# Kernel tuning notes

Measured on AMD Instinct MI355X. Metric: run time of the kernel, lower is better.

## Reference

```python
import math
import jax, jax.numpy as jnp
import numpy as np

BSZ, N_HEADS, N_KV_HEADS, SEQLEN, HEAD_DIM = 1, 32, 8, 2048, 128
DIM = N_HEADS * HEAD_DIM  # 4096
N_REP = N_HEADS // N_KV_HEADS  # 4
NEG = -1e9


def setup_inputs() -> dict:
    key = jax.random.key(0)
    kq, kk, kv = jax.random.split(key, 3)
    q = jax.random.normal(kq, (BSZ, N_HEADS, SEQLEN, HEAD_DIM), dtype=jnp.float32)
    k = jax.random.normal(kk, (BSZ, N_KV_HEADS, SEQLEN, HEAD_DIM), dtype=jnp.float32)
    v = jax.random.normal(kv, (BSZ, N_KV_HEADS, SEQLEN, HEAD_DIM), dtype=jnp.float32)
    # additive causal mask: 0 on/below diagonal, large negative above
    causal = jnp.tril(jnp.ones((SEQLEN, SEQLEN), dtype=bool))
    mask = jnp.where(causal, 0.0, NEG).astype(jnp.float32)
    input_pos = jnp.zeros((1,), dtype=jnp.int64)
    return {"input_pos": input_pos, "q": q, "k": k, "v": v,
            "bsz": BSZ, "seqlen": SEQLEN, "mask": mask}


def reference(input_pos, q, k, v, bsz, seqlen, mask):
    # repeat_kv: (b, n_kv, s, d) -> (b, n_kv*n_rep, s, d), repeat_interleave on head dim
    k = jnp.repeat(k, N_REP, axis=1)
    v = jnp.repeat(v, N_REP, axis=1)
    scale = 1.0 / math.sqrt(q.shape[-1])
    # (b, h, s, s)
    attn = jnp.einsum("bhqd,bhkd->bhqk", q, k) * scale + mask
    attn = jax.nn.softmax(attn, axis=-1)
    y = jnp.einsum("bhqk,bhkd->bhqd", attn, v)  # (b, h, s, d)
    return y.transpose(0, 2, 1, 3).reshape(bsz, seqlen, DIM)
```

## Files before the change

### kernel.cpp

```cpp
#include <hip/hip_runtime.h>
#include <hip/hip_bf16.h>

#define SEQ 2048
#define HD 128
#define NH 32
#define NKV 8
#define ODIM 4096
#define QB 64
#define KVB 64
#define SCALE 0.08838834764831845f
#define NEGBIG -1e9f

typedef __attribute__((ext_vector_type(8))) short bf16x8;
typedef __attribute__((ext_vector_type(4))) float f32x4;

__device__ __forceinline__ unsigned short f2bf(float x) {
  union { __hip_bfloat16 b; unsigned short u; } c;
  c.b = __float2bfloat16(x);
  return c.u;
}

__device__ __forceinline__ unsigned pack2bf(float lo, float hi) {
  union { __hip_bfloat162 h; unsigned u; } c;
  c.h = __float22bfloat162_rn(float2{lo, hi});
  return c.u;
}

__device__ __forceinline__ void gload_lds16(const unsigned char* g, unsigned char* l) {
  __builtin_amdgcn_global_load_lds(
      (const __attribute__((address_space(1))) void*)g,
      (__attribute__((address_space(3))) void*)l, 16, 0, 0);
}

#define KWORK (NKV * SEQ * 16)
#define VWORK (NKV * (SEQ / 2) * 16)
__global__ __launch_bounds__(256) void sdpa_prepass(
    const float* __restrict__ k, const float* __restrict__ v,
    unsigned char* __restrict__ ws) {
  unsigned char* kimg = ws;
  unsigned char* vimg = ws + (NKV * 32 * 16384);
  int idx = (int)blockIdx.x * 256 + (int)threadIdx.x;
  if (idx < KWORK) {
    int hkv = idx >> 15;
    int rem = idx & 32767;
    int rg = rem >> 4;
    int c8 = (rem & 15) << 3;
    const float* src = k + ((size_t)hkv * SEQ + rg) * HD + c8;
    float4 a = *(const float4*)(src);
    float4 b = *(const float4*)(src + 4);
    union { unsigned short hh[8]; uint4 u4; } pk;
    pk.hh[0]=f2bf(a.x); pk.hh[1]=f2bf(a.y); pk.hh[2]=f2bf(a.z); pk.hh[3]=f2bf(a.w);
    pk.hh[4]=f2bf(b.x); pk.hh[5]=f2bf(b.y); pk.hh[6]=f2bf(b.z); pk.hh[7]=f2bf(b.w);
    int t = rg >> 6, r = rg & 63;
    size_t base = ((size_t)(hkv * 32 + t)) << 14;
    *(uint4*)(kimg + base + (r << 8) + ((c8 << 1) ^ ((r & 7) << 4))) = pk.u4;
  } else {
    int u = idx - KWORK;
    if (u >= VWORK) return;
    int hkv = u >> 14;
    int rem = u & 16383;
    int pr = rem >> 4;
    int d0 = (rem & 15) << 3;
    int rg = pr << 1;
    const float* s0 = v + ((size_t)hkv * SEQ + rg) * HD + d0;
    const float* s1 = s0 + HD;
    float4 a0 = *(const float4*)(s0);
    float4 b0 = *(const float4*)(s0 + 4);
    float4 a1 = *(const float4*)(s1);
    float4 b1 = *(const float4*)(s1 + 4);
    float lo[8] = {a0.x,a0.y,a0.z,a0.w,b0.x,b0.y,b0.z,b0.w};
    float hi[8] = {a1.x,a1.y,a1.z,a1.w,b1.x,b1.y,b1.z,b1.w};
    int t = rg >> 6, rr = rg & 63;
    size_t base = ((size_t)(hkv * 32 + t)) << 14;
    int rb = rr << 1;
    #pragma unroll
    for (int j = 0; j < 8; ++j) {
      int d = d0 + j;
      *(unsigned*)(vimg + base + (d << 7) + (rb ^ ((d & 7) << 4))) =
          pack2bf(lo[j], hi[j]);
    }
  }
}

__global__ __launch_bounds__(512, 4) void sdpa_flash_kernel(
    const float* __restrict__ q, const unsigned char* __restrict__ kimg,
    const unsigned char* __restrict__ vimg, float* __restrict__ out) {
  __shared__ __align__(16) unsigned char smem[65536];
  const int tid = threadIdx.x;
  const int w = tid >> 6;
  const int l = tid & 63;
  const int lm = l & 15;
  const int lg = l >> 4;

  const int p = (int)blockIdx.x;
  const int qtA = p;
  const int qtB = 31 - p;
  const int myqt = (w < 4) ? qtA : qtB;
  const int h = (int)blockIdx.y;
  const int hkv = h >> 2;
  const int qbase = myqt * QB + 16 * (w & 3);
  const int myrow = qbase + lm;

  bf16x8 qa[4];
  {
    const float* qr = q + ((size_t)(h * SEQ + myrow)) * HD + 8 * lg;
    #pragma unroll
    for (int c = 0; c < 4; ++c) {
      float4 a = *(const float4*)(qr + 32 * c);
      float4 b = *(const float4*)(qr + 32 * c + 4);
      union { unsigned short hh[8]; bf16x8 vv; } pk;
      pk.hh[0] = f2bf(a.x * SCALE); pk.hh[1] = f2bf(a.y * SCALE);
      pk.hh[2] = f2bf(a.z * SCALE); pk.hh[3] = f2bf(a.w * SCALE);
      pk.hh[4] = f2bf(b.x * SCALE); pk.hh[5] = f2bf(b.y * SCALE);
      pk.hh[6] = f2bf(b.z * SCALE); pk.hh[7] = f2bf(b.w * SCALE);
      qa[c] = pk.vv;
    }
  }

  f32x4 o[8];
  #pragma unroll
  for (int i = 0; i < 8; ++i) o[i] = (f32x4){0.f, 0.f, 0.f, 0.f};
  float mrow = -1e30f;
  float lrow = 0.f;

  const int ntiles = qtB + 1;
  const unsigned char* kt0 = kimg + (((size_t)(hkv * 32)) << 14);
  const unsigned char* vt0 = vimg + (((size_t)(hkv * 32)) << 14);
  const int woff = w << 10;

#define STAGE(tt, bufbase) {                                                 \
    const unsigned char* ks_ = kt0 + (((size_t)(tt)) << 14);                 \
    const unsigned char* vs_ = vt0 + (((size_t)(tt)) << 14);                 \
    unsigned char* Kb_ = (bufbase);                                          \
    unsigned char* Vb_ = (bufbase) + 16384;                                  \
    gload_lds16(ks_ + woff + (l << 4), Kb_ + woff);                          \
    gload_lds16(ks_ + 8192 + woff + (l << 4), Kb_ + 8192 + woff);            \
    gload_lds16(vs_ + woff + (l << 4), Vb_ + woff);                          \
    gload_lds16(vs_ + 8192 + woff + (l << 4), Vb_ + 8192 + woff);            \
  }

  STAGE(0, smem);
  __syncthreads();
  int cur = 0;

  for (int t = 0; t < ntiles; ++t) {
    const int kv0 = t * KVB;
    if (t + 1 < ntiles) STAGE(t + 1, smem + ((cur ^ 1) << 15));

    unsigned char* Klds = smem + (cur << 15);
    unsigned char* Vlds = Klds + 16384;

    if (t <= myqt) {
      f32x4 s[4];
      #pragma unroll
      for (int nt = 0; nt < 4; ++nt) s[nt] = (f32x4){0.f, 0.f, 0.f, 0.f};
      __builtin_amdgcn_s_setprio(1);
      #pragma unroll
      for (int nt = 0; nt < 4; ++nt) {
        int r = (nt << 4) + lm;
        #pragma unroll
        for (int kc = 0; kc < 4; ++kc) {
          int byte = (r << 8) + (((kc << 6) + (lg << 4)) ^ ((r & 7) << 4));
          bf16x8 kb = *(const bf16x8*)(Klds + byte);
          s[nt] = __builtin_amdgcn_mfma_f32_16x16x32_bf16(kb, qa[kc], s[nt], 0, 0, 0);
        }
      }
      __builtin_amdgcn_s_setprio(0);

      if (kv0 + KVB - 1 > qbase) {
        #pragma unroll
        for (int nt = 0; nt < 4; ++nt) {
          #pragma unroll
          for (int i = 0; i < 4; ++i) {
            int col = kv0 + (nt << 4) + (lg << 2) + i;
            s[nt][i] += (col > myrow) ? NEGBIG : 0.f;
          }
        }
      }

      float tm = -1e30f;
      #pragma unroll
      for (int nt = 0; nt < 4; ++nt)
        #pragma unroll
        for (int i = 0; i < 4; ++i) tm = fmaxf(tm, s[nt][i]);
      tm = fmaxf(tm, __shfl_xor(tm, 16));
      tm = fmaxf(tm, __shfl_xor(tm, 32));
      float mn = fmaxf(mrow, tm);
      float fac = __expf(mrow - mn);
      mrow = mn;
      float rs = 0.f;
      #pragma unroll
      for (int nt = 0; nt < 4; ++nt) {
        #pragma unroll
        for (int i = 0; i < 4; ++i) {
          float pv = __expf(s[nt][i] - mn);
          s[nt][i] = pv;
          rs += pv;
        }
      }
      rs += __shfl_xor(rs, 16);
      rs += __shfl_xor(rs, 32);
      lrow = lrow * fac + rs;
      #pragma unroll
      for (int nt2 = 0; nt2 < 8; ++nt2) {
        #pragma unroll
        for (int i = 0; i < 4; ++i) o[nt2][i] *= fac;
      }

      unsigned pk0[4], pk1[4];
      #pragma unroll
      for (int nt = 0; nt < 4; ++nt) {
        pk0[nt] = pack2bf(s[nt][0], s[nt][1]);
        pk1[nt] = pack2bf(s[nt][2], s[nt][3]);
      }
      const int srcA = lm + ((lg & 1) << 5);
      const int srcB = srcA + 16;
      const bool lo2 = (lg < 2);
      bf16x8 pb[2];
      #pragma unroll
      for (int kc = 0; kc < 2; ++kc) {
        int a0 = __shfl((int)pk0[2*kc], srcA), b0 = __shfl((int)pk0[2*kc+1], srcA);
        int a1 = __shfl((int)pk1[2*kc], srcA), b1 = __shfl((int)pk1[2*kc+1], srcA);
        int a2 = __shfl((int)pk0[2*kc], srcB), b2 = __shfl((int)pk0[2*kc+1], srcB);
        int a3 = __shfl((int)pk1[2*kc], srcB), b3 = __shfl((int)pk1[2*kc+1], srcB);
        union { int uu[4]; bf16x8 v; } pw;
        pw.uu[0] = lo2 ? a0 : b0;
        pw.uu[1] = lo2 ? a1 : b1;
        pw.uu[2] = lo2 ? a2 : b2;
        pw.uu[3] = lo2 ? a3 : b3;
        pb[kc] = pw.v;
      }

      __builtin_amdgcn_s_setprio(1);
      #pragma unroll
      for (int nt2 = 0; nt2 < 8; ++nt2) {
        int dr = (nt2 << 4) + lm;
        #pragma unroll
        for (int kc = 0; kc < 2; ++kc) {
          int byte = (dr << 7) + (((kc << 6) + (lg << 4)) ^ ((dr & 7) << 4));
          bf16x8 vb = *(const bf16x8*)(Vlds + byte);
          o[nt2] = __builtin_amdgcn_mfma_f32_16x16x32_bf16(vb, pb[kc], o[nt2], 0, 0, 0);
        }
      }
      __builtin_amdgcn_s_setprio(0);
    }

    __syncthreads();
    cur ^= 1;
  }

  float inv = 1.f / lrow;
  float* orow = out + (size_t)myrow * ODIM + h * HD + (lg << 2);
  #pragma unroll
  for (int nt2 = 0; nt2 < 8; ++nt2) {
    float4 st = {o[nt2][0] * inv, o[nt2][1] * inv, o[nt2][2] * inv, o[nt2][3] * inv};
    *(float4*)(orow + (nt2 << 4)) = st;
  }
#undef STAGE
}

__global__ __launch_bounds__(512, 4) void sdpa_flash_fb(
    const float* __restrict__ q, const float* __restrict__ k,
    const float* __restrict__ v, float* __restrict__ out) {
  __shared__ __align__(16) unsigned char smem[65536];
  const int tid = threadIdx.x;
  const int w = tid >> 6;
  const int l = tid & 63;
  const int lm = l & 15;
  const int lg = l >> 4;
  const int p = (int)blockIdx.x;
  const int qtA = p;
  const int qtB = 31 - p;
  const int myqt = (w < 4) ? qtA : qtB;
  const int h = (int)blockIdx.y;
  const int hkv = h >> 2;
  const int qbase = myqt * QB + 16 * (w & 3);
  const int myrow = qbase + lm;
  bf16x8 qa[4];
  {
    const float* qr = q + ((size_t)(h * SEQ + myrow)) * HD + 8 * lg;
    #pragma unroll
    for (int c = 0; c < 4; ++c) {
      float4 a = *(const float4*)(qr + 32 * c);
      float4 b = *(const float4*)(qr + 32 * c + 4);
      union { unsigned short hh[8]; bf16x8 vv; } pk;
      pk.hh[0] = f2bf(a.x * SCALE); pk.hh[1] = f2bf(a.y * SCALE);
      pk.hh[2] = f2bf(a.z * SCALE); pk.hh[3] = f2bf(a.w * SCALE);
      pk.hh[4] = f2bf(b.x * SCALE); pk.hh[5] = f2bf(b.y * SCALE);
      pk.hh[6] = f2bf(b.z * SCALE); pk.hh[7] = f2bf(b.w * SCALE);
      qa[c] = pk.vv;
    }
  }
  f32x4 o[8];
  #pragma unroll
  for (int i = 0; i < 8; ++i) o[i] = (f32x4){0.f, 0.f, 0.f, 0.f};
  float mrow = -1e30f;
  float lrow = 0.f;
  const int ntiles = qtB + 1;
  const float* kg0 = k + (size_t)hkv * SEQ * HD;
  const float* vg0 = v + (size_t)hkv * SEQ * HD;
  const int k_r0 = tid >> 4;
  const int k_c8 = (tid & 15) << 3;
  const int v_rr = (tid & 31) << 1;
  const int v_d0 = (tid >> 5) << 3;
  float4 ka0, kb0, ka1, kb1, va0, vb0, va1, vb1;
#define LOADT(tt) {                                                          \
    const float* kg_ = kg0 + (size_t)((tt) * KVB) * HD + k_r0 * HD + k_c8;   \
    ka0 = *(const float4*)(kg_);                                             \
    kb0 = *(const float4*)(kg_ + 4);                                         \
    ka1 = *(const float4*)(kg_ + 32 * HD);                                   \
    kb1 = *(const float4*)(kg_ + 32 * HD + 4);                               \
    const float* vg_ = vg0 + (size_t)((tt) * KVB) * HD + v_rr * HD + v_d0;   \
    va0 = *(const float4*)(vg_);                                             \
    vb0 = *(const float4*)(vg_ + 4);                                         \
    va1 = *(const float4*)(vg_ + HD);                                        \
    vb1 = *(const float4*)(vg_ + HD + 4);                                    \
  }
#define WRITELDS(bufbase) {                                                  \
    unsigned char* Kb_ = (bufbase);                                          \
    unsigned char* Vb_ = (bufbase) + 16384;                                  \
    {                                                                        \
      union { unsigned short hh[8]; uint4 u4; } pk_;                         \
      pk_.hh[0]=f2bf(ka0.x); pk_.hh[1]=f2bf(ka0.y);                          \
      pk_.hh[2]=f2bf(ka0.z); pk_.hh[3]=f2bf(ka0.w);                          \
      pk_.hh[4]=f2bf(kb0.x); pk_.hh[5]=f2bf(kb0.y);                          \
      pk_.hh[6]=f2bf(kb0.z); pk_.hh[7]=f2bf(kb0.w);                          \
      int byte_ = (k_r0 << 8) + ((k_c8 << 1) ^ ((k_r0 & 7) << 4));           \
      *(uint4*)(Kb_ + byte_) = pk_.u4;                                       \
    }                                                                        \
    {                                                                        \
      int r1_ = k_r0 + 32;                                                   \
      union { unsigned short hh[8]; uint4 u4; } pk_;                         \
      pk_.hh[0]=f2bf(ka1.x); pk_.hh[1]=f2bf(ka1.y);                          \
      pk_.hh[2]=f2bf(ka1.z); pk_.hh[3]=f2bf(ka1.w);                          \
      pk_.hh[4]=f2bf(kb1.x); pk_.hh[5]=f2bf(kb1.y);                          \
      pk_.hh[6]=f2bf(kb1.z); pk_.hh[7]=f2bf(kb1.w);                          \
      int byte_ = (r1_ << 8) + ((k_c8 << 1) ^ ((r1_ & 7) << 4));             \
      *(uint4*)(Kb_ + byte_) = pk_.u4;                                       \
    }                                                                        \
    {                                                                        \
      unsigned w0_ = pack2bf(va0.x, va1.x), w1_ = pack2bf(va0.y, va1.y);     \
      unsigned w2_ = pack2bf(va0.z, va1.z), w3_ = pack2bf(va0.w, va1.w);     \
      unsigned w4_ = pack2bf(vb0.x, vb1.x), w5_ = pack2bf(vb0.y, vb1.y);     \
      unsigned w6_ = pack2bf(vb0.z, vb1.z), w7_ = pack2bf(vb0.w, vb1.w);     \
      int rb_ = v_rr << 1;                                                   \
      int d_;                                                                \
      d_ = v_d0;     *(unsigned*)(Vb_ + (d_ << 7) + (rb_ ^ ((d_ & 7) << 4))) = w0_; \
      d_ = v_d0 + 1; *(unsigned*)(Vb_ + (d_ << 7) + (rb_ ^ ((d_ & 7) << 4))) = w1_; \
      d_ = v_d0 + 2; *(unsigned*)(Vb_ + (d_ << 7) + (rb_ ^ ((d_ & 7) << 4))) = w2_; \
      d_ = v_d0 + 3; *(unsigned*)(Vb_ + (d_ << 7) + (rb_ ^ ((d_ & 7) << 4))) = w3_; \
      d_ = v_d0 + 4; *(unsigned*)(Vb_ + (d_ << 7) + (rb_ ^ ((d_ & 7) << 4))) = w4_; \
      d_ = v_d0 + 5; *(unsigned*)(Vb_ + (d_ << 7) + (rb_ ^ ((d_ & 7) << 4))) = w5_; \
      d_ = v_d0 + 6; *(unsigned*)(Vb_ + (d_ << 7) + (rb_ ^ ((d_ & 7) << 4))) = w6_; \
      d_ = v_d0 + 7; *(unsigned*)(Vb_ + (d_ << 7) + (rb_ ^ ((d_ & 7) << 4))) = w7_; \
    }                                                                        \
  }
  LOADT(0);
  WRITELDS(smem);
  __syncthreads();
  int cur = 0;
  for (int t = 0; t < ntiles; ++t) {
    const int kv0 = t * KVB;
    const bool have_next = (t + 1 < ntiles);
    if (have_next) LOADT(t + 1);
    unsigned char* Klds = smem + (cur << 15);
    unsigned char* Vlds = Klds + 16384;
    if (t <= myqt) {
      f32x4 s[4];
      #pragma unroll
      for (int nt = 0; nt < 4; ++nt) s[nt] = (f32x4){0.f, 0.f, 0.f, 0.f};
      #pragma unroll
      for (int nt = 0; nt < 4; ++nt) {
        int r = (nt << 4) + lm;
        #pragma unroll
        for (int kc = 0; kc < 4; ++kc) {
          int byte = (r << 8) + (((kc << 6) + (lg << 4)) ^ ((r & 7) << 4));
          bf16x8 kb = *(const bf16x8*)(Klds + byte);
          s[nt] = __builtin_amdgcn_mfma_f32_16x16x32_bf16(kb, qa[kc], s[nt], 0, 0, 0);
        }
      }
      if (kv0 + KVB - 1 > qbase) {
        #pragma unroll
        for (int nt = 0; nt < 4; ++nt) {
          #pragma unroll
          for (int i = 0; i < 4; ++i) {
            int col = kv0 + (nt << 4) + (lg << 2) + i;
            s[nt][i] += (col > myrow) ? NEGBIG : 0.f;
          }
        }
      }
      float tm = -1e30f;
      #pragma unroll
      for (int nt = 0; nt < 4; ++nt)
        #pragma unroll
        for (int i = 0; i < 4; ++i) tm = fmaxf(tm, s[nt][i]);
      tm = fmaxf(tm, __shfl_xor(tm, 16));
      tm = fmaxf(tm, __shfl_xor(tm, 32));
      float mn = fmaxf(mrow, tm);
      float fac = __expf(mrow - mn);
      mrow = mn;
      float rs = 0.f;
      #pragma unroll
      for (int nt = 0; nt < 4; ++nt) {
        #pragma unroll
        for (int i = 0; i < 4; ++i) {
          float pv = __expf(s[nt][i] - mn);
          s[nt][i] = pv;
          rs += pv;
        }
      }
      rs += __shfl_xor(rs, 16);
      rs += __shfl_xor(rs, 32);
      lrow = lrow * fac + rs;
      #pragma unroll
      for (int nt2 = 0; nt2 < 8; ++nt2) {
        #pragma unroll
        for (int i = 0; i < 4; ++i) o[nt2][i] *= fac;
      }
      unsigned pk0[4], pk1[4];
      #pragma unroll
      for (int nt = 0; nt < 4; ++nt) {
        pk0[nt] = pack2bf(s[nt][0], s[nt][1]);
        pk1[nt] = pack2bf(s[nt][2], s[nt][3]);
      }
      const int srcA = lm + ((lg & 1) << 5);
      const int srcB = srcA + 16;
      const bool lo2 = (lg < 2);
      bf16x8 pb[2];
      #pragma unroll
      for (int kc = 0; kc < 2; ++kc) {
        int a0 = __shfl((int)pk0[2*kc], srcA), b0 = __shfl((int)pk0[2*kc+1], srcA);
        int a1 = __shfl((int)pk1[2*kc], srcA), b1 = __shfl((int)pk1[2*kc+1], srcA);
        int a2 = __shfl((int)pk0[2*kc], srcB), b2 = __shfl((int)pk0[2*kc+1], srcB);
        int a3 = __shfl((int)pk1[2*kc], srcB), b3 = __shfl((int)pk1[2*kc+1], srcB);
        union { int uu[4]; bf16x8 v; } pw;
        pw.uu[0] = lo2 ? a0 : b0;
        pw.uu[1] = lo2 ? a1 : b1;
        pw.uu[2] = lo2 ? a2 : b2;
        pw.uu[3] = lo2 ? a3 : b3;
        pb[kc] = pw.v;
      }
      #pragma unroll
      for (int nt2 = 0; nt2 < 8; ++nt2) {
        int dr = (nt2 << 4) + lm;
        #pragma unroll
        for (int kc = 0; kc < 2; ++kc) {
          int byte = (dr << 7) + (((kc << 6) + (lg << 4)) ^ ((dr & 7) << 4));
          bf16x8 vb = *(const bf16x8*)(Vlds + byte);
          o[nt2] = __builtin_amdgcn_mfma_f32_16x16x32_bf16(vb, pb[kc], o[nt2], 0, 0, 0);
        }
      }
    }
    if (have_next) {
      WRITELDS(smem + ((cur ^ 1) << 15));
    }
    __syncthreads();
    cur ^= 1;
  }
  float inv = 1.f / lrow;
  float* orow = out + (size_t)myrow * ODIM + h * HD + (lg << 2);
  #pragma unroll
  for (int nt2 = 0; nt2 < 8; ++nt2) {
    float4 st = {o[nt2][0] * inv, o[nt2][1] * inv, o[nt2][2] * inv, o[nt2][3] * inv};
    *(float4*)(orow + (nt2 << 4)) = st;
  }
#undef LOADT
#undef WRITELDS
}

extern "C" void kernel_launch(void* const* d_in, const int* in_sizes, int n_in,
                              void* d_out, int out_size, void* d_ws, size_t ws_size,
                              hipStream_t stream) {
  const float* q = (const float*)d_in[1];
  const float* k = (const float*)d_in[2];
  const float* v = (const float*)d_in[3];
  float* out = (float*)d_out;
  dim3 grid(SEQ / QB / 2, NH);
  const size_t need = (size_t)(NKV * 32 * 16384) * 2;
  if (ws_size >= need && d_ws != nullptr) {
    unsigned char* ws = (unsigned char*)d_ws;
    int total = KWORK + VWORK;
    sdpa_prepass<<<(total + 255) / 256, 256, 0, stream>>>(k, v, ws);
    sdpa_flash_kernel<<<grid, 512, 0, stream>>>(
        q, ws, ws + (NKV * 32 * 16384), out);
  } else {
    sdpa_flash_fb<<<grid, 512, 0, stream>>>(q, k, v, out);
  }
}
```

Before: 86.26 us.

## Switch flash attention to 32x32x16 MFMA with 4 waves and lazy rescaling

```diff
diff --git a/kernel.cpp b/kernel.cpp
--- a/kernel.cpp
+++ b/kernel.cpp
@@ -13,6 +13,8 @@
 
 typedef __attribute__((ext_vector_type(8))) short bf16x8;
 typedef __attribute__((ext_vector_type(4))) float f32x4;
+typedef __attribute__((ext_vector_type(16))) float f32x16;
+typedef __attribute__((ext_vector_type(2))) int i32x2;
 
 __device__ __forceinline__ unsigned short f2bf(float x) {
   union { __hip_bfloat16 b; unsigned short u; } c;
@@ -82,61 +84,66 @@
   }
 }
 
-__global__ __launch_bounds__(512, 4) void sdpa_flash_kernel(
+__global__ __launch_bounds__(256, 2) void sdpa_flash_kernel(
     const float* __restrict__ q, const unsigned char* __restrict__ kimg,
     const unsigned char* __restrict__ vimg, float* __restrict__ out) {
   __shared__ __align__(16) unsigned char smem[65536];
   const int tid = threadIdx.x;
   const int w = tid >> 6;
   const int l = tid & 63;
-  const int lm = l & 15;
-  const int lg = l >> 4;
+  const int q31 = l & 31;
+  const int hi = l >> 5;
 
   const int p = (int)blockIdx.x;
-  const int qtA = p;
-  const int qtB = 31 - p;
-  const int myqt = (w < 4) ? qtA : qtB;
+  const int qtA = p, qtB = 31 - p;
+  const int myqt = (w < 2) ? qtA : qtB;
   const int h = (int)blockIdx.y;
   const int hkv = h >> 2;
-  const int qbase = myqt * QB + 16 * (w & 3);
-  const int myrow = qbase + lm;
-
-  bf16x8 qa[4];
+  const int qbase = myqt * QB + 32 * (w & 1);
+  const int myq = qbase + q31;
+
+  bf16x8 qa[8];
   {
-    const float* qr = q + ((size_t)(h * SEQ + myrow)) * HD + 8 * lg;
+    const float* qr = q + ((size_t)(h * SEQ + myq)) * HD + 8 * hi;
     #pragma unroll
-    for (int c = 0; c < 4; ++c) {
-      float4 a = *(const float4*)(qr + 32 * c);
-      float4 b = *(const float4*)(qr + 32 * c + 4);
+    for (int s = 0; s < 8; ++s) {
+      float4 a = *(const float4*)(qr + 16 * s);
+      float4 b = *(const float4*)(qr + 16 * s + 4);
       union { unsigned short hh[8]; bf16x8 vv; } pk;
       pk.hh[0] = f2bf(a.x * SCALE); pk.hh[1] = f2bf(a.y * SCALE);
       pk.hh[2] = f2bf(a.z * SCALE); pk.hh[3] = f2bf(a.w * SCALE);
       pk.hh[4] = f2bf(b.x * SCALE); pk.hh[5] = f2bf(b.y * SCALE);
       pk.hh[6] = f2bf(b.z * SCALE); pk.hh[7] = f2bf(b.w * SCALE);
-      qa[c] = pk.vv;
-    }
-  }
-
-  f32x4 o[8];
+      qa[s] = pk.vv;
+    }
+  }
+
+  f32x16 o[4];
   #pragma unroll
-  for (int i = 0; i < 8; ++i) o[i] = (f32x4){0.f, 0.f, 0.f, 0.f};
-  float mrow = -1e30f;
-  float lrow = 0.f;
+  for (int db = 0; db < 4; ++db)
+    #pragma unroll
+    for (int r = 0; r < 16; ++r) o[db][r] = 0.f;
+  float mrow = -1e30f, lrow = 0.f;
 
   const int ntiles = qtB + 1;
   const unsigned char* kt0 = kimg + (((size_t)(hkv * 32)) << 14);
   const unsigned char* vt0 = vimg + (((size_t)(hkv * 32)) << 14);
-  const int woff = w << 10;
-
-#define STAGE(tt, bufbase) {                                                 \
-    const unsigned char* ks_ = kt0 + (((size_t)(tt)) << 14);                 \
-    const unsigned char* vs_ = vt0 + (((size_t)(tt)) << 14);                 \
-    unsigned char* Kb_ = (bufbase);                                          \
-    unsigned char* Vb_ = (bufbase) + 16384;                                  \
-    gload_lds16(ks_ + woff + (l << 4), Kb_ + woff);                          \
-    gload_lds16(ks_ + 8192 + woff + (l << 4), Kb_ + 8192 + woff);            \
-    gload_lds16(vs_ + woff + (l << 4), Vb_ + woff);                          \
-    gload_lds16(vs_ + 8192 + woff + (l << 4), Vb_ + 8192 + woff);            \
+
+#define STAGE(tt, bufbase) {                                   \
+    const unsigned char* ks_ = kt0 + (((size_t)(tt)) << 14);   \
+    const unsigned char* vs_ = vt0 + (((size_t)(tt)) << 14);   \
+    unsigned char* Kb_ = (bufbase) + (w << 12);                \
+    unsigned char* Vb_ = (bufbase) + 16384 + (w << 12);        \
+    const unsigned char* kso_ = ks_ + (w << 12) + (l << 4);    \
+    const unsigned char* vso_ = vs_ + (w << 12) + (l << 4);    \
+    gload_lds16(kso_, Kb_);                                    \
+    gload_lds16(kso_ + 1024, Kb_ + 1024);                      \
+    gload_lds16(kso_ + 2048, Kb_ + 2048);                      \
+    gload_lds16(kso_ + 3072, Kb_ + 3072);                      \
+    gload_lds16(vso_, Vb_);                                    \
+    gload_lds16(vso_ + 1024, Vb_ + 1024);                      \
+    gload_lds16(vso_ + 2048, Vb_ + 2048);                      \
+    gload_lds16(vso_ + 3072, Vb_ + 3072);                      \
   }
 
   STAGE(0, smem);
@@ -151,95 +158,93 @@
     unsigned char* Vlds = Klds + 16384;
 
     if (t <= myqt) {
-      f32x4 s[4];
-      #pragma unroll
-      for (int nt = 0; nt < 4; ++nt) s[nt] = (f32x4){0.f, 0.f, 0.f, 0.f};
+      f32x16 s0, s1;
+      #pragma unroll
+      for (int r = 0; r < 16; ++r) { s0[r] = 0.f; s1[r] = 0.f; }
       __builtin_amdgcn_s_setprio(1);
       #pragma unroll
-      for (int nt = 0; nt < 4; ++nt) {
-        int r = (nt << 4) + lm;
-        #pragma unroll
-        for (int kc = 0; kc < 4; ++kc) {
-          int byte = (r << 8) + (((kc << 6) + (lg << 4)) ^ ((r & 7) << 4));
-          bf16x8 kb = *(const bf16x8*)(Klds + byte);
-          s[nt] = __builtin_amdgcn_mfma_f32_16x16x32_bf16(kb, qa[kc], s[nt], 0, 0, 0);
-        }
+      for (int s = 0; s < 8; ++s) {
+        int colb = 32 * s + 16 * hi;
+        int r0 = q31;
+        bf16x8 k0 = *(const bf16x8*)(Klds + (r0 << 8) + (colb ^ ((r0 & 7) << 4)));
+        int r1 = 32 + q31;
+        bf16x8 k1 = *(const bf16x8*)(Klds + (r1 << 8) + (colb ^ ((r1 & 7) << 4)));
+        s0 = __builtin_amdgcn_mfma_f32_32x32x16_bf16(k0, qa[s], s0, 0, 0, 0);
+        s1 = __builtin_amdgcn_mfma_f32_32x32x16_bf16(k1, qa[s], s1, 0, 0, 0);
       }
       __builtin_amdgcn_s_setprio(0);
 
-      if (kv0 + KVB - 1 > qbase) {
-        #pragma unroll
-        for (int nt = 0; nt < 4; ++nt) {
-          #pragma unroll
-          for (int i = 0; i < 4; ++i) {
-            int col = kv0 + (nt << 4) + (lg << 2) + i;
-            s[nt][i] += (col > myrow) ? NEGBIG : 0.f;
-          }
+      if (t == myqt) {
+        #pragma unroll
+        for (int r = 0; r < 16; ++r) {
+          int kvr = kv0 + (r & 3) + 8 * (r >> 2) + 4 * hi;
+          s0[r] += (kvr > myq) ? NEGBIG : 0.f;
+          s1[r] += (kvr + 32 > myq) ? NEGBIG : 0.f;
         }
       }
 
       float tm = -1e30f;
       #pragma unroll
-      for (int nt = 0; nt < 4; ++nt)
-        #pragma unroll
-        for (int i = 0; i < 4; ++i) tm = fmaxf(tm, s[nt][i]);
-      tm = fmaxf(tm, __shfl_xor(tm, 16));
+      for (int r = 0; r < 16; ++r) {
+        tm = fmaxf(tm, s0[r]);
+        tm = fmaxf(tm, s1[r]);
+      }
       tm = fmaxf(tm, __shfl_xor(tm, 32));
       float mn = fmaxf(mrow, tm);
-      float fac = __expf(mrow - mn);
-      mrow = mn;
+      if (!__all(tm <= mrow + 8.0f)) {
+        float fac = __expf(mrow - mn);
+        mrow = mn;
+        lrow *= fac;
+        #pragma unroll
+        for (int db = 0; db < 4; ++db)
+          #pragma unroll
+          for (int r = 0; r < 16; ++r) o[db][r] *= fac;
+      }
       float rs = 0.f;
       #pragma unroll
-      for (int nt = 0; nt < 4; ++nt) {
-        #pragma unroll
-        for (int i = 0; i < 4; ++i) {
-          float pv = __expf(s[nt][i] - mn);
-          s[nt][i] = pv;
-          rs += pv;
-        }
-      }
-      rs += __shfl_xor(rs, 16);
+      for (int r = 0; r < 16; ++r) {
+        s0[r] = __expf(s0[r] - mrow); rs += s0[r];
+        s1[r] = __expf(s1[r] - mrow); rs += s1[r];
+      }
       rs += __shfl_xor(rs, 32);
-      lrow = lrow * fac + rs;
-      #pragma unroll
-      for (int nt2 = 0; nt2 < 8; ++nt2) {
-        #pragma unroll
-        for (int i = 0; i < 4; ++i) o[nt2][i] *= fac;
-      }
-
-      unsigned pk0[4], pk1[4];
-      #pragma unroll
-      for (int nt = 0; nt < 4; ++nt) {
-        pk0[nt] = pack2bf(s[nt][0], s[nt][1]);
-        pk1[nt] = pack2bf(s[nt][2], s[nt][3]);
-      }
-      const int srcA = lm + ((lg & 1) << 5);
-      const int srcB = srcA + 16;
-      const bool lo2 = (lg < 2);
-      bf16x8 pb[2];
-      #pragma unroll
-      for (int kc = 0; kc < 2; ++kc) {
-        int a0 = __shfl((int)pk0[2*kc], srcA), b0 = __shfl((int)pk0[2*kc+1], srcA);
-        int a1 = __shfl((int)pk1[2*kc], srcA), b1 = __shfl((int)pk1[2*kc+1], srcA);
-        int a2 = __shfl((int)pk0[2*kc], srcB), b2 = __shfl((int)pk0[2*kc+1], srcB);
-        int a3 = __shfl((int)pk1[2*kc], srcB), b3 = __shfl((int)pk1[2*kc+1], srcB);
-        union { int uu[4]; bf16x8 v; } pw;
-        pw.uu[0] = lo2 ? a0 : b0;
-        pw.uu[1] = lo2 ? a1 : b1;
-        pw.uu[2] = lo2 ? a2 : b2;
-        pw.uu[3] = lo2 ? a3 : b3;
-        pb[kc] = pw.v;
+      lrow += rs;
+
+      bf16x8 pf[4];
+      #pragma unroll
+      for (int s2 = 0; s2 < 2; ++s2) {
+        {
+          unsigned a0 = pack2bf(s0[8*s2+0], s0[8*s2+1]);
+          unsigned a1 = pack2bf(s0[8*s2+2], s0[8*s2+3]);
+          unsigned b0 = pack2bf(s0[8*s2+4], s0[8*s2+5]);
+          unsigned b1 = pack2bf(s0[8*s2+6], s0[8*s2+7]);
+          i32x2 r0 = __builtin_amdgcn_permlane32_swap((int)a0, (int)b0, false, false);
+          i32x2 r1 = __builtin_amdgcn_permlane32_swap((int)a1, (int)b1, false, false);
+          union { int u[4]; bf16x8 v; } pw;
+          pw.u[0] = r0.x; pw.u[1] = r1.x; pw.u[2] = r0.y; pw.u[3] = r1.y;
+          pf[s2] = pw.v;
+        }
+        {
+          unsigned a0 = pack2bf(s1[8*s2+0], s1[8*s2+1]);
+          unsigned a1 = pack2bf(s1[8*s2+2], s1[8*s2+3]);
+          unsigned b0 = pack2bf(s1[8*s2+4], s1[8*s2+5]);
+          unsigned b1 = pack2bf(s1[8*s2+6], s1[8*s2+7]);
+          i32x2 r0 = __builtin_amdgcn_permlane32_swap((int)a0, (int)b0, false, false);
+          i32x2 r1 = __builtin_amdgcn_permlane32_swap((int)a1, (int)b1, false, false);
+          union { int u[4]; bf16x8 v; } pw;
+          pw.u[0] = r0.x; pw.u[1] = r1.x; pw.u[2] = r0.y; pw.u[3] = r1.y;
+          pf[2 + s2] = pw.v;
+        }
       }
 
       __builtin_amdgcn_s_setprio(1);
       #pragma unroll
-      for (int nt2 = 0; nt2 < 8; ++nt2) {
-        int dr = (nt2 << 4) + lm;
-        #pragma unroll
-        for (int kc = 0; kc < 2; ++kc) {
-          int byte = (dr << 7) + (((kc << 6) + (lg << 4)) ^ ((dr & 7) << 4));
-          bf16x8 vb = *(const bf16x8*)(Vlds + byte);
-          o[nt2] = __builtin_amdgcn_mfma_f32_16x16x32_bf16(vb, pb[kc], o[nt2], 0, 0, 0);
+      for (int s = 0; s < 4; ++s) {
+        int colb = 32 * s + 16 * hi;
+        #pragma unroll
+        for (int db = 0; db < 4; ++db) {
+          int dd = db * 32 + q31;
+          bf16x8 vf = *(const bf16x8*)(Vlds + (dd << 7) + (colb ^ ((dd & 7) << 4)));
+          o[db] = __builtin_amdgcn_mfma_f32_32x32x16_bf16(vf, pf[s], o[db], 0, 0, 0);
         }
       }
       __builtin_amdgcn_s_setprio(0);
@@ -250,11 +255,16 @@
   }
 
   float inv = 1.f / lrow;
-  float* orow = out + (size_t)myrow * ODIM + h * HD + (lg << 2);
+  float* obase = out + (size_t)myq * ODIM + h * HD;
   #pragma unroll
-  for (int nt2 = 0; nt2 < 8; ++nt2) {
-    float4 st = {o[nt2][0] * inv, o[nt2][1] * inv, o[nt2][2] * inv, o[nt2][3] * inv};
-    *(float4*)(orow + (nt2 << 4)) = st;
+  for (int db = 0; db < 4; ++db) {
+    #pragma unroll
+    for (int c = 0; c < 4; ++c) {
+      int d0 = db * 32 + 8 * c + 4 * hi;
+      float4 st = {o[db][4*c+0] * inv, o[db][4*c+1] * inv,
+                   o[db][4*c+2] * inv, o[db][4*c+3] * inv};
+      *(float4*)(obase + d0) = st;
+    }
   }
 #undef STAGE
 }
@@ -481,7 +491,7 @@
     unsigned char* ws = (unsigned char*)d_ws;
     int total = KWORK + VWORK;
     sdpa_prepass<<<(total + 255) / 256, 256, 0, stream>>>(k, v, ws);
-    sdpa_flash_kernel<<<grid, 512, 0, stream>>>(
+    sdpa_flash_kernel<<<grid, 256, 0, stream>>>(
         q, ws, ws + (NKV * 32 * 16384), out);
   } else {
     sdpa_flash_fb<<<grid, 512, 0, stream>>>(q, k, v, out);
```

New measurement: 91.90 us. 6.5% more time.
